# Performance work log

Hardware: AMD Instinct MI355X
Metric: run time of the kernel (lower is better)

The kernel has to match this reference:

```python
import jax, jax.numpy as jnp
import numpy as np

EPS = 1e-5

def _layernorm(x, g, b):
    mu = jnp.mean(x, axis=-1, keepdims=True)
    var = jnp.mean(jnp.square(x - mu), axis=-1, keepdims=True)
    return (x - mu) * jax.lax.rsqrt(var + EPS) * g + b

def setup_inputs() -> dict:
    key = jax.random.key(0)
    ks = jax.random.split(key, 4)
    E, B, D, H = 8, 131072, 128, 128
    features = jax.random.normal(ks[0], (E, B, D), dtype=jnp.float32)
    gate_w1 = jax.random.normal(ks[1], (E * D, H), dtype=jnp.float32) * (1.0 / np.sqrt(E * D))
    gate_b1 = jnp.zeros((H,), dtype=jnp.float32)
    ln1_g = jnp.ones((H,), dtype=jnp.float32)
    ln1_b = jnp.zeros((H,), dtype=jnp.float32)
    gate_w2 = jax.random.normal(ks[2], (H, E), dtype=jnp.float32) * (1.0 / np.sqrt(H))
    gate_b2 = jnp.zeros((E,), dtype=jnp.float32)
    out_g = jnp.ones((D,), dtype=jnp.float32)
    out_b = jnp.zeros((D,), dtype=jnp.float32)
    return {"features": features, "gate_w1": gate_w1, "gate_b1": gate_b1,
            "ln1_g": ln1_g, "ln1_b": ln1_b, "gate_w2": gate_w2, "gate_b2": gate_b2,
            "out_g": out_g, "out_b": out_b}

def reference(features, gate_w1, gate_b1, ln1_g, ln1_b, gate_w2, gate_b2, out_g, out_b):
    # features: [E, B, D]
    E, B, D = features.shape
    # concat teacher features per sample -> [B, E*D]
    concat = jnp.transpose(features, (1, 0, 2)).reshape(B, E * D)
    h = concat @ gate_w1 + gate_b1                       # [B, 128]
    h = jax.nn.gelu(h, approximate=False)                # torch nn.GELU default = exact
    h = _layernorm(h, ln1_g, ln1_b)
    logits = h @ gate_w2 + gate_b2                       # [B, E]
    scores = jax.nn.softmax(logits, axis=-1)             # [B, E]
    # per-expert scalar weight then LayerNorm over D
    weighted = scores.T[:, :, None] * features           # [E, B, D]
    out = _layernorm(weighted, out_g, out_b)             # [E, B, D]
    return out
```

## Files before the change

kernel.cpp:

```cpp
#include <hip/hip_runtime.h>
#include <hip/hip_bf16.h>

#define B_N   131072
#define E_N   8
#define D_N   128
#define H_N   128
#define K_N   1024
#define MBLK  16
#define NTHR  256

typedef __attribute__((ext_vector_type(8))) short bf16x8;
typedef __attribute__((ext_vector_type(4))) float f32x4;
typedef __attribute__((ext_vector_type(4))) unsigned short u16x4;

__device__ __forceinline__ unsigned short f2bf(float f) {
    union { float f; unsigned int i; } c; c.f = f;
    unsigned int x = c.i;
    return (unsigned short)((x + 0x7fffu + ((x >> 16) & 1u)) >> 16);
}
__device__ __forceinline__ float bf2f(unsigned short u) {
    union { unsigned int i; float f; } c; c.i = ((unsigned int)u) << 16; return c.f;
}

__global__ void prep_w1_frags(const float* __restrict__ w1,
                              unsigned short* __restrict__ frag) {
    int t    = blockIdx.x * blockDim.x + threadIdx.x;
    int lane = t & 63;
    int fgi  = t >> 6;
    int kst  = fgi >> 3;
    int nt   = fgi & 7;
    int n    = nt * 16 + (lane & 15);
    int k0   = kst * 32 + (lane >> 4) * 8;
    bf16x8 v;
    #pragma unroll
    for (int j = 0; j < 8; ++j)
        v[j] = (short)f2bf(w1[(k0 + j) * H_N + n]);
    *reinterpret_cast<bf16x8*>(frag + (size_t)t * 8) = v;
}

__global__ __launch_bounds__(NTHR, 4)
void moe_fused(const float* __restrict__ feats,
               const unsigned short* __restrict__ w1frag,
               const float* __restrict__ gate_b1,
               const float* __restrict__ ln1_g,
               const float* __restrict__ ln1_b,
               const float* __restrict__ gate_w2,
               const float* __restrict__ gate_b2,
               const float* __restrict__ out_g,
               const float* __restrict__ out_b,
               float* __restrict__ out)
{
    __shared__ __attribute__((aligned(16))) unsigned short featS[MBLK * K_N];
    __shared__ __attribute__((aligned(16))) unsigned short hSb[MBLK * 136];
    __shared__ float scoreS[MBLK * E_N];

    const int tid = threadIdx.x;
    const int b0  = blockIdx.x * MBLK;

    #pragma unroll
    for (int e = 0; e < E_N; ++e) {
        const f32x4* src = reinterpret_cast<const f32x4*>(
            feats + ((size_t)e * B_N + b0) * D_N);
        #pragma unroll
        for (int i = 0; i < (MBLK * D_N / 4) / NTHR; ++i) {
            int f   = tid + i * NTHR;
            f32x4 v = src[f];
            int m   = f >> 5;
            int dq  = f & 31;
            int k   = e * D_N + dq * 4;
            int uoff = m * K_N + ((((k >> 3) ^ (m & 7)) << 3) | (k & 7));
            u16x4 u;
            u[0] = f2bf(v[0]); u[1] = f2bf(v[1]);
            u[2] = f2bf(v[2]); u[3] = f2bf(v[3]);
            *reinterpret_cast<u16x4*>(&featS[uoff]) = u;
        }
    }
    __syncthreads();

    const int wv   = tid >> 6;
    const int lane = tid & 63;
    const int lrow = lane & 15;
    const int lkh  = lane >> 4;
    const int nt0  = wv * 2, nt1 = nt0 + 1;
    f32x4 acc0 = {0.f, 0.f, 0.f, 0.f};
    f32x4 acc1 = {0.f, 0.f, 0.f, 0.f};
    const bf16x8* wf = reinterpret_cast<const bf16x8*>(w1frag);
    const int arow = lrow * K_N;
    const int asw  = lrow & 7;
    #pragma unroll 4
    for (int kk = 0; kk < 32; ++kk) {
        bf16x8 a  = *reinterpret_cast<const bf16x8*>(
            &featS[arow + ((((kk << 2) + lkh) ^ asw) << 3)]);
        bf16x8 b0 = wf[((kk * 8 + nt0) << 6) + lane];
        bf16x8 b1 = wf[((kk * 8 + nt1) << 6) + lane];
        acc0 = __builtin_amdgcn_mfma_f32_16x16x32_bf16(a, b0, acc0, 0, 0, 0);
        acc1 = __builtin_amdgcn_mfma_f32_16x16x32_bf16(a, b1, acc1, 0, 0, 0);
    }

    {
        const int colA = nt0 * 16 + lrow;
        const int colB = nt1 * 16 + lrow;
        const float bA = gate_b1[colA];
        const float bB = gate_b1[colB];
        #pragma unroll
        for (int r = 0; r < 4; ++r) {
            int row  = lkh * 4 + r;
            float vA = acc0[r] + bA;
            float vB = acc1[r] + bB;
            vA = 0.5f * vA * (1.f + erff(vA * 0.70710678118654752f));
            vB = 0.5f * vB * (1.f + erff(vB * 0.70710678118654752f));
            hSb[row * 136 + colA] = f2bf(vA);
            hSb[row * 136 + colB] = f2bf(vB);
        }
    }
    __syncthreads();

    {
        const int row = tid >> 4;
        const int gl  = tid & 15;
        bf16x8 h8 = *reinterpret_cast<const bf16x8*>(&hSb[row * 136 + gl * 8]);
        float hv[8];
        #pragma unroll
        for (int j = 0; j < 8; ++j) hv[j] = bf2f((unsigned short)h8[j]);
        float s = 0.f, sq = 0.f;
        #pragma unroll
        for (int j = 0; j < 8; ++j) { s += hv[j]; sq += hv[j] * hv[j]; }
        #pragma unroll
        for (int msk = 1; msk < 16; msk <<= 1) {
            s  += __shfl_xor(s, msk);
            sq += __shfl_xor(sq, msk);
        }
        float mu  = s * (1.f / 128.f);
        float var = sq * (1.f / 128.f) - mu * mu;
        float rs  = rsqrtf(var + 1e-5f);
        const f32x4* lgv = reinterpret_cast<const f32x4*>(ln1_g + gl * 8);
        const f32x4* lbv = reinterpret_cast<const f32x4*>(ln1_b + gl * 8);
        f32x4 lg0 = lgv[0], lg1 = lgv[1];
        f32x4 lb0 = lbv[0], lb1 = lbv[1];
        float p[8] = {0.f, 0.f, 0.f, 0.f, 0.f, 0.f, 0.f, 0.f};
        #pragma unroll
        for (int j = 0; j < 8; ++j) {
            int col  = gl * 8 + j;
            float g  = (j < 4) ? lg0[j & 3] : lg1[j & 3];
            float bb = (j < 4) ? lb0[j & 3] : lb1[j & 3];
            float hn = (hv[j] - mu) * rs * g + bb;
            const f32x4* w2v = reinterpret_cast<const f32x4*>(gate_w2 + col * 8);
            f32x4 wa = w2v[0], wb = w2v[1];
            #pragma unroll
            for (int e = 0; e < 4; ++e) p[e]     += hn * wa[e];
            #pragma unroll
            for (int e = 0; e < 4; ++e) p[e + 4] += hn * wb[e];
        }
        #pragma unroll
        for (int msk = 1; msk < 16; msk <<= 1) {
            #pragma unroll
            for (int e = 0; e < 8; ++e) p[e] += __shfl_xor(p[e], msk);
        }
        float lg[8], mx = -3.0e38f;
        #pragma unroll
        for (int e = 0; e < 8; ++e) { lg[e] = p[e] + gate_b2[e]; mx = fmaxf(mx, lg[e]); }
        float den = 0.f, ex[8];
        #pragma unroll
        for (int e = 0; e < 8; ++e) { ex[e] = __expf(lg[e] - mx); den += ex[e]; }
        float inv = 1.f / den;
        if (gl < 8) scoreS[row * 8 + gl] = ex[gl] * inv;
    }
    __syncthreads();

    {
        const int m  = tid >> 4;
        const int gl = tid & 15;
        const f32x4* ogv = reinterpret_cast<const f32x4*>(out_g + gl * 8);
        const f32x4* obv = reinterpret_cast<const f32x4*>(out_b + gl * 8);
        f32x4 og0 = ogv[0], og1 = ogv[1];
        f32x4 ob0 = obv[0], ob1 = obv[1];
        #pragma unroll
        for (int e = 0; e < E_N; ++e) {
            int slot = ((e << 4) | gl) ^ (m & 7);
            bf16x8 x8 = *reinterpret_cast<const bf16x8*>(&featS[m * K_N + (slot << 3)]);
            float x[8];
            #pragma unroll
            for (int j = 0; j < 8; ++j) x[j] = bf2f((unsigned short)x8[j]);
            float s = 0.f, sq = 0.f;
            #pragma unroll
            for (int j = 0; j < 8; ++j) { s += x[j]; sq += x[j] * x[j]; }
            #pragma unroll
            for (int msk = 1; msk < 16; msk <<= 1) {
                s  += __shfl_xor(s, msk);
                sq += __shfl_xor(sq, msk);
            }
            float mu  = s * (1.f / 128.f);
            float var = sq * (1.f / 128.f) - mu * mu;
            float sc  = scoreS[m * 8 + e];
            float srs = sc * rsqrtf(sc * sc * var + 1e-5f);
            float* dst = out + ((size_t)e * B_N + b0 + m) * D_N + gl * 8;
            f32x4 o0, o1;
            #pragma unroll
            for (int j = 0; j < 4; ++j)
                o0[j] = (x[j] - mu) * srs * og0[j] + ob0[j];
            #pragma unroll
            for (int j = 0; j < 4; ++j)
                o1[j] = (x[4 + j] - mu) * srs * og1[j] + ob1[j];
            *reinterpret_cast<f32x4*>(dst)     = o0;
            *reinterpret_cast<f32x4*>(dst + 4) = o1;
        }
    }
}

extern "C" void kernel_launch(void* const* d_in, const int* in_sizes, int n_in,
                              void* d_out, int out_size, void* d_ws, size_t ws_size,
                              hipStream_t stream) {
    const float* feats   = (const float*)d_in[0];
    const float* gate_w1 = (const float*)d_in[1];
    const float* gate_b1 = (const float*)d_in[2];
    const float* ln1_g   = (const float*)d_in[3];
    const float* ln1_b   = (const float*)d_in[4];
    const float* gate_w2 = (const float*)d_in[5];
    const float* gate_b2 = (const float*)d_in[6];
    const float* out_g   = (const float*)d_in[7];
    const float* out_b   = (const float*)d_in[8];
    float* outp = (float*)d_out;
    unsigned short* frag = (unsigned short*)d_ws;

    prep_w1_frags<<<64, NTHR, 0, stream>>>(gate_w1, frag);
    moe_fused<<<B_N / MBLK, NTHR, 0, stream>>>(
        feats, frag, gate_b1, ln1_g, ln1_b, gate_w2, gate_b2, out_g, out_b, outp);
}
```

Measured before the change: 308.4 us.

## Double rows per block, split waves over row tiles, prefetch W1 fragments

The block now handles 32 rows with 512 threads, and the 8 waves are split into 2 row tiles times 4 column pairs. Each W1 fragment fetched from global memory therefore serves twice as many rows. All eight expert feature loads are issued together before converting and staging into LDS, and the next k-step's W1 fragments are prefetched into registers during the MFMA loop. The cost is twice the LDS per block (64KB), which limits how many blocks fit on a CU. The launch bound of 512 threads with 4 blocks also constrains register allocation and could cause spills.

```diff
diff --git a/kernel.cpp b/kernel.cpp
--- a/kernel.cpp
+++ b/kernel.cpp
@@ -6,8 +6,8 @@
 #define D_N   128
 #define H_N   128
 #define K_N   1024
-#define MBLK  16
-#define NTHR  256
+#define MBLK  32
+#define NTHR  512
 
 typedef __attribute__((ext_vector_type(8))) short bf16x8;
 typedef __attribute__((ext_vector_type(4))) float f32x4;
@@ -58,17 +58,26 @@
     const int b0  = blockIdx.x * MBLK;
 
     #pragma unroll
-    for (int e = 0; e < E_N; ++e) {
-        const f32x4* src = reinterpret_cast<const f32x4*>(
-            feats + ((size_t)e * B_N + b0) * D_N);
-        #pragma unroll
-        for (int i = 0; i < (MBLK * D_N / 4) / NTHR; ++i) {
-            int f   = tid + i * NTHR;
-            f32x4 v = src[f];
-            int m   = f >> 5;
-            int dq  = f & 31;
-            int k   = e * D_N + dq * 4;
-            int uoff = m * K_N + ((((k >> 3) ^ (m & 7)) << 3) | (k & 7));
+    for (int i = 0; i < 2; ++i) {
+        const int f  = tid + i * NTHR;
+        const int m  = f >> 5;
+        const int dq = f & 31;
+        f32x4 v0 = reinterpret_cast<const f32x4*>(feats + ((size_t)0 * B_N + b0) * D_N)[f];
+        f32x4 v1 = reinterpret_cast<const f32x4*>(feats + ((size_t)1 * B_N + b0) * D_N)[f];
+        f32x4 v2 = reinterpret_cast<const f32x4*>(feats + ((size_t)2 * B_N + b0) * D_N)[f];
+        f32x4 v3 = reinterpret_cast<const f32x4*>(feats + ((size_t)3 * B_N + b0) * D_N)[f];
+        f32x4 v4 = reinterpret_cast<const f32x4*>(feats + ((size_t)4 * B_N + b0) * D_N)[f];
+        f32x4 v5 = reinterpret_cast<const f32x4*>(feats + ((size_t)5 * B_N + b0) * D_N)[f];
+        f32x4 v6 = reinterpret_cast<const f32x4*>(feats + ((size_t)6 * B_N + b0) * D_N)[f];
+        f32x4 v7 = reinterpret_cast<const f32x4*>(feats + ((size_t)7 * B_N + b0) * D_N)[f];
+        const int sw = (m & 7);
+        const int mb = m * K_N;
+        #pragma unroll
+        for (int e = 0; e < 8; ++e) {
+            f32x4 v = (e == 0) ? v0 : (e == 1) ? v1 : (e == 2) ? v2 : (e == 3) ? v3
+                    : (e == 4) ? v4 : (e == 5) ? v5 : (e == 6) ? v6 : v7;
+            int k    = e * D_N + dq * 4;
+            int uoff = mb + ((((k >> 3) ^ sw) << 3) | (k & 7));
             u16x4 u;
             u[0] = f2bf(v[0]); u[1] = f2bf(v[1]);
             u[2] = f2bf(v[2]); u[3] = f2bf(v[3]);
@@ -81,20 +90,28 @@
     const int lane = tid & 63;
     const int lrow = lane & 15;
     const int lkh  = lane >> 4;
-    const int nt0  = wv * 2, nt1 = nt0 + 1;
+    const int rt   = wv >> 2;
+    const int nq   = wv & 3;
+    const int nt0  = nq * 2, nt1 = nt0 + 1;
     f32x4 acc0 = {0.f, 0.f, 0.f, 0.f};
     f32x4 acc1 = {0.f, 0.f, 0.f, 0.f};
     const bf16x8* wf = reinterpret_cast<const bf16x8*>(w1frag);
-    const int arow = lrow * K_N;
+    const int arow = (rt * 16 + lrow) * K_N;
     const int asw  = lrow & 7;
-    #pragma unroll 4
+    bf16x8 b0c = wf[((0 * 8 + nt0) << 6) + lane];
+    bf16x8 b1c = wf[((0 * 8 + nt1) << 6) + lane];
+    #pragma unroll
     for (int kk = 0; kk < 32; ++kk) {
-        bf16x8 a  = *reinterpret_cast<const bf16x8*>(
+        bf16x8 b0n, b1n;
+        if (kk < 31) {
+            b0n = wf[(((kk + 1) * 8 + nt0) << 6) + lane];
+            b1n = wf[(((kk + 1) * 8 + nt1) << 6) + lane];
+        }
+        bf16x8 a = *reinterpret_cast<const bf16x8*>(
             &featS[arow + ((((kk << 2) + lkh) ^ asw) << 3)]);
-        bf16x8 b0 = wf[((kk * 8 + nt0) << 6) + lane];
-        bf16x8 b1 = wf[((kk * 8 + nt1) << 6) + lane];
-        acc0 = __builtin_amdgcn_mfma_f32_16x16x32_bf16(a, b0, acc0, 0, 0, 0);
-        acc1 = __builtin_amdgcn_mfma_f32_16x16x32_bf16(a, b1, acc1, 0, 0, 0);
+        acc0 = __builtin_amdgcn_mfma_f32_16x16x32_bf16(a, b0c, acc0, 0, 0, 0);
+        acc1 = __builtin_amdgcn_mfma_f32_16x16x32_bf16(a, b1c, acc1, 0, 0, 0);
+        b0c = b0n; b1c = b1n;
     }
 
     {
@@ -104,7 +121,7 @@
         const float bB = gate_b1[colB];
         #pragma unroll
         for (int r = 0; r < 4; ++r) {
-            int row  = lkh * 4 + r;
+            int row  = rt * 16 + lkh * 4 + r;
             float vA = acc0[r] + bA;
             float vB = acc1[r] + bB;
             vA = 0.5f * vA * (1.f + erff(vA * 0.70710678118654752f));
@@ -222,7 +239,7 @@
     float* outp = (float*)d_out;
     unsigned short* frag = (unsigned short*)d_ws;
 
-    prep_w1_frags<<<64, NTHR, 0, stream>>>(gate_w1, frag);
+    prep_w1_frags<<<64, 256, 0, stream>>>(gate_w1, frag);
     moe_fused<<<B_N / MBLK, NTHR, 0, stream>>>(
         feats, frag, gate_b1, ln1_g, ln1_b, gate_w2, gate_b2, out_g, out_b, outp);
 }
```

Result: no change. 303.9 us (-1.4%).
